# Performance work log

Measured on AMD Instinct MI355X. Metric: run time of the kernel, lower is better.

The kernel has to match this reference:

```python
import jax, jax.numpy as jnp
import numpy as np

B, P, S, D, H, DFF, F, FIN = 16, 25, 1024, 128, 8, 512, 1, 4
SIGMA, OMEGA = 0.1, 0.5
DH = D // H


def setup_inputs() -> dict:
    key = jax.random.key(0)
    ks = jax.random.split(key, 16)
    s = lambda i, sh, sc=1.0: jax.random.normal(ks[i], sh, dtype=jnp.float32) * sc
    return dict(
        x=s(0, (B, P, D)),
        y=s(1, (B, FIN, 1)),
        K=s(2, (B, P, S, D), 0.02),
        V=s(3, (B, P, S, D), 0.02),
        w=jnp.ones((B, P, 1), jnp.float32) / P,
        I=jax.random.randint(ks[4], (B, P, S), 0, P, dtype=jnp.int32),
        Wq=s(5, (D, D), 0.05), Wk=s(6, (D, D), 0.05),
        Wv=s(7, (D, D), 0.05), Wo=s(8, (D, D), 0.05),
        W1=s(9, (D, DFF), 0.05), b1=jnp.zeros((DFF,), jnp.float32),
        W2=s(10, (DFF, D), 0.05), b2=jnp.zeros((D,), jnp.float32),
        Wout=s(11, (D, F), 0.05), bout=jnp.zeros((F,), jnp.float32),
        eps_k=s(12, (B, P, 1, D)), eps_v=s(13, (B, P, 1, D)), eps_z=s(14, (B, P, 1, D)),
        t=512,
    )


def reference(x, y, K, V, w, I, Wq, Wk, Wv, Wo, W1, b1, W2, b2, Wout, bout,
              eps_k, eps_v, eps_z, t):
    # ---- MultiHeadAttention_SMC: per-particle self-attention with reparam noise ----
    xq = x[:, :, None, :]                                   # (B,P,1,D)
    q = xq @ Wq                                             # (B,P,1,D)
    k = xq @ Wk + SIGMA * eps_k                             # noisy key particle
    v = xq @ Wv + SIGMA * eps_v                             # noisy value particle
    K = K.at[:, :, t, :].set(k[:, :, 0, :])                 # write current step into state
    V = V.at[:, :, t, :].set(v[:, :, 0, :])
    q_h = q.reshape(B, P, 1, H, DH)
    K_h = K.reshape(B, P, S, H, DH)
    V_h = V.reshape(B, P, S, H, DH)
    scores = jnp.einsum('bpqhd,bpshd->bphqs', q_h, K_h) / jnp.sqrt(jnp.float32(DH))
    valid = (jnp.arange(S) <= t)[None, None, None, None, :]  # attend to steps <= t
    scores = jnp.where(valid, scores, jnp.float32(-1e9))
    attn = jax.nn.softmax(scores, axis=-1)                  # (B,P,H,1,S)
    ctx = jnp.einsum('bphqs,bpshd->bpqhd', attn, V_h).reshape(B, P, 1, D)
    z = ctx @ Wo + SIGMA * eps_z                            # reparametrized attention output

    # ---- FFN + output layer (dropout is identity at inference) ----
    r_ = jax.nn.relu(z @ W1 + b1) @ W2 + b2                 # (B,P,1,D)
    pred = r_ @ Wout + bout                                 # (B,P,1,F)

    p_t = pred[:, :, 0, :]                                  # (B,P,F)
    y_sq = y[..., 0]                                        # (B,FIN)
    y_t = jnp.broadcast_to(y_sq[:, None, 0:1], (B, P, F))   # target_feature = 0
    mu = y_t - p_t                                          # (B,P,F)
    log_w_full = jnp.einsum('bpf,bqf->bpq', mu, mu) * (-0.5 * OMEGA)
    log_w = jnp.diagonal(log_w_full, axis1=1, axis2=2)      # (B,P)
    log_w = log_w - jnp.min(log_w, axis=-1, keepdims=True)
    w_new = jnp.exp(log_w)
    w_new = w_new / jnp.sum(w_new, axis=1, keepdims=True)
    w_new = jax.lax.stop_gradient(w_new)

    # ---- particle resampling: categorical sample + gather on particle axis ----
    idx = jax.random.categorical(jax.random.key(42),
                                 jnp.log(w_new + 1e-10)[:, None, :],
                                 axis=-1, shape=(B, P))     # (B,P) ancestor indices
    K_res = jnp.take_along_axis(K, idx[:, :, None, None], axis=1)
    V_res = jnp.take_along_axis(V, idx[:, :, None, None], axis=1)
    I_res = jnp.take_along_axis(I, idx[:, :, None], axis=1)
    I_new = I_res.at[:, :, t].set(idx.astype(I.dtype))
    return (r_, z, pred, w_new[..., None], K_res, V_res, I_new)
```

## Files before the change

kernel.cpp:

```cpp
#include <hip/hip_runtime.h>
#include <math.h>

#define B_ 16
#define P_ 25
#define S_ 1024
#define D_ 128
#define H_ 8
#define DH_ 16
#define DFF_ 512
#define SIGMA_ 0.1f


__global__ __launch_bounds__(128) void qkv_kernel(
    const float* __restrict__ x, const float* __restrict__ Wq,
    const float* __restrict__ Wk, const float* __restrict__ Wv,
    const float* __restrict__ eps_k, const float* __restrict__ eps_v,
    float* __restrict__ q, float* __restrict__ k, float* __restrict__ v) {
  int bp = blockIdx.x;
  int d = threadIdx.x;
  __shared__ float xs[D_];
  xs[d] = x[bp * D_ + d];
  __syncthreads();
  float accq = 0.f, acck = 0.f, accv = 0.f;
  for (int i = 0; i < D_; ++i) {
    float xv = xs[i];
    accq += xv * Wq[i * D_ + d];
    acck += xv * Wk[i * D_ + d];
    accv += xv * Wv[i * D_ + d];
  }
  q[bp * D_ + d] = accq;
  k[bp * D_ + d] = acck + SIGMA_ * eps_k[bp * D_ + d];
  v[bp * D_ + d] = accv + SIGMA_ * eps_v[bp * D_ + d];
}

__global__ __launch_bounds__(512) void attn_kernel(
    const float* __restrict__ q, const float* __restrict__ kn,
    const float* __restrict__ vn, const float* __restrict__ K,
    const float* __restrict__ V, const int* __restrict__ tptr,
    float* __restrict__ ctx) {
  int bp = blockIdx.x;
  int t = tptr[0];
  int tid = threadIdx.x;
  int wave = tid >> 6;
  int lane = tid & 63;
  __shared__ float qs[D_];
  __shared__ float accs[8][D_];
  __shared__ float ms[8][H_];
  __shared__ float ls[8][H_];
  if (tid < D_) qs[tid] = q[bp * D_ + tid] * 0.25f;
  __syncthreads();
  const float* Kb = K + (size_t)bp * S_ * D_;
  const float* Vb = V + (size_t)bp * S_ * D_;
  float m = -1e30f, l = 0.f, a0 = 0.f, a1 = 0.f;
  float q0 = qs[2 * lane], q1 = qs[2 * lane + 1];
  for (int s = wave; s <= t; s += 8) {
    const float* Kr, *Vr;
    if (s == t) { Kr = kn + bp * D_; Vr = vn + bp * D_; }
    else        { Kr = Kb + (size_t)s * D_; Vr = Vb + (size_t)s * D_; }
    float2 kk = *(const float2*)(Kr + 2 * lane);
    float2 vv = *(const float2*)(Vr + 2 * lane);
    float p = q0 * kk.x + q1 * kk.y;
    p += __shfl_xor(p, 1);
    p += __shfl_xor(p, 2);
    p += __shfl_xor(p, 4);
    float mnew = fmaxf(m, p);
    float scale = expf(m - mnew);
    float e = expf(p - mnew);
    l = l * scale + e;
    a0 = a0 * scale + e * vv.x;
    a1 = a1 * scale + e * vv.y;
    m = mnew;
  }
  accs[wave][2 * lane] = a0;
  accs[wave][2 * lane + 1] = a1;
  if ((lane & 7) == 0) { ms[wave][lane >> 3] = m; ls[wave][lane >> 3] = l; }
  __syncthreads();
  if (tid < D_) {
    int h = tid >> 4;
    float mg = -1e30f;
    for (int w2 = 0; w2 < 8; ++w2) mg = fmaxf(mg, ms[w2][h]);
    float L = 0.f, C = 0.f;
    for (int w2 = 0; w2 < 8; ++w2) {
      float sc = expf(ms[w2][h] - mg);
      L += ls[w2][h] * sc;
      C += accs[w2][tid] * sc;
    }
    ctx[bp * D_ + tid] = C / L;
  }
}

__global__ __launch_bounds__(512) void head_kernel(
    const float* __restrict__ ctx, const float* __restrict__ Wo,
    const float* __restrict__ eps_z, const float* __restrict__ W1,
    const float* __restrict__ b1, const float* __restrict__ W2,
    const float* __restrict__ b2, const float* __restrict__ Wout,
    const float* __restrict__ bout, float* __restrict__ out_r,
    float* __restrict__ out_z, float* __restrict__ out_pred) {
  int bp = blockIdx.x;
  int tid = threadIdx.x;
  __shared__ float cs[D_];
  __shared__ float zs[D_];
  __shared__ float as[DFF_];
  __shared__ float rs[D_];
  if (tid < D_) cs[tid] = ctx[bp * D_ + tid];
  __syncthreads();
  if (tid < D_) {
    float acc = 0.f;
    for (int i = 0; i < D_; ++i) acc += cs[i] * Wo[i * D_ + tid];
    acc += SIGMA_ * eps_z[bp * D_ + tid];
    zs[tid] = acc;
    out_z[bp * D_ + tid] = acc;
  }
  __syncthreads();
  {
    float acc = b1[tid];
    for (int i = 0; i < D_; ++i) acc += zs[i] * W1[i * DFF_ + tid];
    as[tid] = fmaxf(acc, 0.f);
  }
  __syncthreads();
  if (tid < D_) {
    float acc = b2[tid];
    for (int j = 0; j < DFF_; ++j) acc += as[j] * W2[j * D_ + tid];
    rs[tid] = acc;
    out_r[bp * D_ + tid] = acc;
  }
  __syncthreads();
  if (tid < 64) {
    float acc = rs[tid] * Wout[tid] + rs[tid + 64] * Wout[tid + 64];
    acc += __shfl_xor(acc, 1);
    acc += __shfl_xor(acc, 2);
    acc += __shfl_xor(acc, 4);
    acc += __shfl_xor(acc, 8);
    acc += __shfl_xor(acc, 16);
    acc += __shfl_xor(acc, 32);
    if (tid == 0) out_pred[bp] = acc + bout[0];
  }
}

__device__ inline unsigned rotl_(unsigned x, int r) {
  return (x << r) | (x >> (32 - r));
}

__device__ inline void threefry2x32_(unsigned x0, unsigned x1, unsigned& o0,
                                     unsigned& o1) {
  const unsigned k0 = 0u, k1 = 42u;
  const unsigned k2 = k0 ^ k1 ^ 0x1BD11BDAu;
  x0 += k0; x1 += k1;
#define RND_(r) { x0 += x1; x1 = rotl_(x1, r); x1 ^= x0; }
  RND_(13) RND_(15) RND_(26) RND_(6)   x0 += k1; x1 += k2 + 1u;
  RND_(17) RND_(29) RND_(16) RND_(24)  x0 += k2; x1 += k0 + 2u;
  RND_(13) RND_(15) RND_(26) RND_(6)   x0 += k0; x1 += k1 + 3u;
  RND_(17) RND_(29) RND_(16) RND_(24)  x0 += k1; x1 += k2 + 4u;
  RND_(13) RND_(15) RND_(26) RND_(6)   x0 += k2; x1 += k0 + 5u;
#undef RND_
  o0 = x0; o1 = x1;
}

__device__ inline float gumbel_at_(int n) {
  unsigned o0, o1;
  threefry2x32_(0u, (unsigned)n, o0, o1);
  unsigned bits = o0 ^ o1;
  unsigned fb = (bits >> 9) | 0x3f800000u;
  float f = __uint_as_float(fb) - 1.0f;
  const float tiny = 1.1754944e-38f;
  float u = fmaxf(tiny, f * (1.0f - tiny) + tiny);
  return -logf(-logf(u));
}

__global__ __launch_bounds__(64) void sample_kernel(
    const float* __restrict__ pred, const float* __restrict__ y,
    float* __restrict__ out_w, int* __restrict__ idx) {
  int b = blockIdx.x;
  int tid = threadIdx.x;
  __shared__ float lw[P_];
  __shared__ float logits[P_];
  __shared__ float red[2];
  if (tid < P_) {
    float mu = y[b * 4] - pred[b * P_ + tid];
    lw[tid] = -0.25f * (mu * mu);
  }
  __syncthreads();
  if (tid == 0) {
    float mn = lw[0];
    for (int p = 1; p < P_; ++p) mn = fminf(mn, lw[p]);
    red[0] = mn;
  }
  __syncthreads();
  if (tid < P_) lw[tid] = expf(lw[tid] - red[0]);
  __syncthreads();
  if (tid == 0) {
    float s = 0.f;
    for (int p = 0; p < P_; ++p) s += lw[p];
    red[1] = s;
  }
  __syncthreads();
  if (tid < P_) {
    float wn = lw[tid] / red[1];
    out_w[b * P_ + tid] = wn;
    logits[tid] = logf(wn + 1e-10f);
  }
  __syncthreads();
  if (tid < P_) {
    float best = -1e30f;
    int bestj = 0;
    for (int j = 0; j < P_; ++j) {
      int n = (b * P_ + tid) * P_ + j;
      float val = gumbel_at_(n) + logits[j];
      if (val > best) { best = val; bestj = j; }
    }
    idx[b * P_ + tid] = bestj;
  }
}

__global__ __launch_bounds__(256) void gather_kernel(
    const float* __restrict__ K, const float* __restrict__ V,
    const float* __restrict__ kn, const float* __restrict__ vn,
    const int* __restrict__ idx, const int* __restrict__ tptr,
    float* __restrict__ outK, float* __restrict__ outV) {
  const int CH = 4;
  const int F4 = (S_ * D_ / 4) / CH;
  int bid = blockIdx.x;
  int tv = bid / (B_ * P_ * CH);
  int rem = bid - tv * (B_ * P_ * CH);
  int bp = rem / CH;
  int chunk = rem - bp * CH;
  int b = bp / P_;
  int j = idx[bp];
  int t = tptr[0];
  const float* src = (tv == 0 ? K : V) + (size_t)(b * P_ + j) * (S_ * D_);
  const float4* sub = (const float4*)((tv == 0 ? kn : vn) + (b * P_ + j) * D_);
  float* dst = (tv == 0 ? outK : outV) + (size_t)bp * (S_ * D_);
  const float4* src4 = (const float4*)src;
  float4* dst4 = (float4*)dst;
  int base = chunk * F4;
  int tlo = t * (D_ / 4);
  for (int i = base + threadIdx.x; i < base + F4; i += 256) {
    float4 val;
    if (i >= tlo && i < tlo + D_ / 4) val = sub[i - tlo];
    else                              val = src4[i];
    dst4[i] = val;
  }
}

__global__ __launch_bounds__(256) void inew_kernel(
    const int* __restrict__ I, const int* __restrict__ idx,
    const int* __restrict__ tptr, float* __restrict__ outI) {
  int bp = blockIdx.x;
  int b = bp / P_;
  int j = idx[bp];
  int t = tptr[0];
  const int* src = I + (b * P_ + j) * S_;
  float* dst = outI + bp * S_;
  for (int s = threadIdx.x; s < S_; s += 256) {
    int val = (s == t) ? j : src[s];
    dst[s] = (float)val;
  }
}

extern "C" void kernel_launch(void* const* d_in, const int* in_sizes, int n_in,
                              void* d_out, int out_size, void* d_ws,
                              size_t ws_size, hipStream_t stream) {
  const float* x     = (const float*)d_in[0];
  const float* y     = (const float*)d_in[1];
  const float* K     = (const float*)d_in[2];
  const float* V     = (const float*)d_in[3];
  const int*   I     = (const int*)d_in[5];
  const float* Wq    = (const float*)d_in[6];
  const float* Wk    = (const float*)d_in[7];
  const float* Wv    = (const float*)d_in[8];
  const float* Wo    = (const float*)d_in[9];
  const float* W1    = (const float*)d_in[10];
  const float* b1    = (const float*)d_in[11];
  const float* W2    = (const float*)d_in[12];
  const float* b2    = (const float*)d_in[13];
  const float* Wout  = (const float*)d_in[14];
  const float* bout  = (const float*)d_in[15];
  const float* eps_k = (const float*)d_in[16];
  const float* eps_v = (const float*)d_in[17];
  const float* eps_z = (const float*)d_in[18];
  const int*   tptr  = (const int*)d_in[19];

  float* out      = (float*)d_out;
  float* out_r    = out;
  float* out_z    = out + 51200;
  float* out_pred = out + 102400;
  float* out_w    = out + 102800;
  float* outK     = out + 103200;
  float* outV     = outK + (size_t)52428800;
  float* outI     = outV + (size_t)52428800;

  float* ws  = (float*)d_ws;
  float* q   = ws;
  float* k   = ws + 51200;
  float* v   = ws + 102400;
  float* ctx = ws + 153600;
  int*   idx = (int*)(ws + 204800);

  qkv_kernel<<<B_ * P_, 128, 0, stream>>>(x, Wq, Wk, Wv, eps_k, eps_v, q, k, v);
  attn_kernel<<<B_ * P_, 512, 0, stream>>>(q, k, v, K, V, tptr, ctx);
  head_kernel<<<B_ * P_, 512, 0, stream>>>(ctx, Wo, eps_z, W1, b1, W2, b2, Wout,
                                           bout, out_r, out_z, out_pred);
  sample_kernel<<<B_, 64, 0, stream>>>(out_pred, y, out_w, idx);
  gather_kernel<<<B_ * P_ * 4 * 2, 256, 0, stream>>>(K, V, k, v, idx, tptr,
                                                     outK, outV);
  inew_kernel<<<B_ * P_, 256, 0, stream>>>(I, idx, tptr, outI);
}
```

Measured before the change: 792.6 us.

## Vectorize attention loads, split head matvecs, use nontemporal stores in gather

The attention kernel now loads K/V rows as float4 with half-waves, so each wave processes two sequence rows per iteration and there are sixteen partial softmax states to merge instead of eight. The head kernel splits the Wo and W2 matvecs across all 512 threads with partial sums reduced through shared memory. The gather and I-copy kernels use nontemporal stores to avoid polluting cache with the large K/V resample output. The changes are independent and mainly target memory bandwidth on the copy-dominated path.

```diff
diff --git a/kernel.cpp b/kernel.cpp
--- a/kernel.cpp
+++ b/kernel.cpp
@@ -9,6 +9,8 @@
 #define DH_ 16
 #define DFF_ 512
 #define SIGMA_ 0.1f
+
+typedef float f4 __attribute__((ext_vector_type(4)));
 
 
 __global__ __launch_bounds__(128) void qkv_kernel(
@@ -43,44 +45,51 @@
   int tid = threadIdx.x;
   int wave = tid >> 6;
   int lane = tid & 63;
-  __shared__ float qs[D_];
-  __shared__ float accs[8][D_];
-  __shared__ float ms[8][H_];
-  __shared__ float ls[8][H_];
+  int row = lane >> 5;
+  int lr = lane & 31;
+  int w16 = wave * 2 + row;
+  __shared__ __align__(16) float qs[D_];
+  __shared__ __align__(16) float accs[16][D_];
+  __shared__ float ms[16][H_];
+  __shared__ float ls[16][H_];
   if (tid < D_) qs[tid] = q[bp * D_ + tid] * 0.25f;
   __syncthreads();
-  const float* Kb = K + (size_t)bp * S_ * D_;
-  const float* Vb = V + (size_t)bp * S_ * D_;
-  float m = -1e30f, l = 0.f, a0 = 0.f, a1 = 0.f;
-  float q0 = qs[2 * lane], q1 = qs[2 * lane + 1];
-  for (int s = wave; s <= t; s += 8) {
-    const float* Kr, *Vr;
-    if (s == t) { Kr = kn + bp * D_; Vr = vn + bp * D_; }
-    else        { Kr = Kb + (size_t)s * D_; Vr = Vb + (size_t)s * D_; }
-    float2 kk = *(const float2*)(Kr + 2 * lane);
-    float2 vv = *(const float2*)(Vr + 2 * lane);
-    float p = q0 * kk.x + q1 * kk.y;
+  const f4* Kb = (const f4*)(K + (size_t)bp * S_ * D_);
+  const f4* Vb = (const f4*)(V + (size_t)bp * S_ * D_);
+  const f4* kn4 = (const f4*)(kn + bp * D_);
+  const f4* vn4 = (const f4*)(vn + bp * D_);
+  f4 qv = *(const f4*)(qs + 4 * lr);
+  float m = -1e30f, l = 0.f;
+  f4 acc = {0.f, 0.f, 0.f, 0.f};
+  const int RD4 = D_ / 4;
+  for (int s = w16; s <= t; s += 16) {
+    const f4 *Kr, *Vr;
+    if (s == t) { Kr = kn4; Vr = vn4; }
+    else        { Kr = Kb + (size_t)s * RD4; Vr = Vb + (size_t)s * RD4; }
+    f4 kk = Kr[lr];
+    f4 vv = Vr[lr];
+    float p = qv.x * kk.x + qv.y * kk.y + qv.z * kk.z + qv.w * kk.w;
     p += __shfl_xor(p, 1);
     p += __shfl_xor(p, 2);
-    p += __shfl_xor(p, 4);
     float mnew = fmaxf(m, p);
     float scale = expf(m - mnew);
     float e = expf(p - mnew);
     l = l * scale + e;
-    a0 = a0 * scale + e * vv.x;
-    a1 = a1 * scale + e * vv.y;
+    acc.x = acc.x * scale + e * vv.x;
+    acc.y = acc.y * scale + e * vv.y;
+    acc.z = acc.z * scale + e * vv.z;
+    acc.w = acc.w * scale + e * vv.w;
     m = mnew;
   }
-  accs[wave][2 * lane] = a0;
-  accs[wave][2 * lane + 1] = a1;
-  if ((lane & 7) == 0) { ms[wave][lane >> 3] = m; ls[wave][lane >> 3] = l; }
+  *(f4*)(&accs[w16][4 * lr]) = acc;
+  if ((lr & 3) == 0) { ms[w16][lr >> 2] = m; ls[w16][lr >> 2] = l; }
   __syncthreads();
   if (tid < D_) {
     int h = tid >> 4;
     float mg = -1e30f;
-    for (int w2 = 0; w2 < 8; ++w2) mg = fmaxf(mg, ms[w2][h]);
+    for (int w2 = 0; w2 < 16; ++w2) mg = fmaxf(mg, ms[w2][h]);
     float L = 0.f, C = 0.f;
-    for (int w2 = 0; w2 < 8; ++w2) {
+    for (int w2 = 0; w2 < 16; ++w2) {
       float sc = expf(ms[w2][h] - mg);
       L += ls[w2][h] * sc;
       C += accs[w2][tid] * sc;
@@ -98,31 +107,46 @@
     float* __restrict__ out_z, float* __restrict__ out_pred) {
   int bp = blockIdx.x;
   int tid = threadIdx.x;
+  int d = tid & 127;
+  int qq = tid >> 7;
   __shared__ float cs[D_];
   __shared__ float zs[D_];
-  __shared__ float as[DFF_];
+  __shared__ float as_[DFF_];
   __shared__ float rs[D_];
+  __shared__ float part[4][D_];
   if (tid < D_) cs[tid] = ctx[bp * D_ + tid];
   __syncthreads();
+  {
+    float acc = 0.f;
+    int i0 = qq * 32;
+    for (int i = i0; i < i0 + 32; ++i) acc += cs[i] * Wo[i * D_ + d];
+    part[qq][d] = acc;
+  }
+  __syncthreads();
   if (tid < D_) {
-    float acc = 0.f;
-    for (int i = 0; i < D_; ++i) acc += cs[i] * Wo[i * D_ + tid];
-    acc += SIGMA_ * eps_z[bp * D_ + tid];
-    zs[tid] = acc;
-    out_z[bp * D_ + tid] = acc;
+    float z = part[0][tid] + part[1][tid] + part[2][tid] + part[3][tid] +
+              SIGMA_ * eps_z[bp * D_ + tid];
+    zs[tid] = z;
+    out_z[bp * D_ + tid] = z;
   }
   __syncthreads();
   {
     float acc = b1[tid];
     for (int i = 0; i < D_; ++i) acc += zs[i] * W1[i * DFF_ + tid];
-    as[tid] = fmaxf(acc, 0.f);
+    as_[tid] = fmaxf(acc, 0.f);
+  }
+  __syncthreads();
+  {
+    float acc = 0.f;
+    int j0 = qq * 128;
+    for (int j = j0; j < j0 + 128; ++j) acc += as_[j] * W2[j * D_ + d];
+    part[qq][d] = acc;
   }
   __syncthreads();
   if (tid < D_) {
-    float acc = b2[tid];
-    for (int j = 0; j < DFF_; ++j) acc += as[j] * W2[j * D_ + tid];
-    rs[tid] = acc;
-    out_r[bp * D_ + tid] = acc;
+    float r = part[0][tid] + part[1][tid] + part[2][tid] + part[3][tid] + b2[tid];
+    rs[tid] = r;
+    out_r[bp * D_ + tid] = r;
   }
   __syncthreads();
   if (tid < 64) {
@@ -228,17 +252,17 @@
   int j = idx[bp];
   int t = tptr[0];
   const float* src = (tv == 0 ? K : V) + (size_t)(b * P_ + j) * (S_ * D_);
-  const float4* sub = (const float4*)((tv == 0 ? kn : vn) + (b * P_ + j) * D_);
+  const f4* sub = (const f4*)((tv == 0 ? kn : vn) + (b * P_ + j) * D_);
   float* dst = (tv == 0 ? outK : outV) + (size_t)bp * (S_ * D_);
-  const float4* src4 = (const float4*)src;
-  float4* dst4 = (float4*)dst;
+  const f4* src4 = (const f4*)src;
+  f4* dst4 = (f4*)dst;
   int base = chunk * F4;
   int tlo = t * (D_ / 4);
   for (int i = base + threadIdx.x; i < base + F4; i += 256) {
-    float4 val;
+    f4 val;
     if (i >= tlo && i < tlo + D_ / 4) val = sub[i - tlo];
     else                              val = src4[i];
-    dst4[i] = val;
+    __builtin_nontemporal_store(val, dst4 + i);
   }
 }
 
@@ -253,7 +277,7 @@
   float* dst = outI + bp * S_;
   for (int s = threadIdx.x; s < S_; s += 256) {
     int val = (s == t) ? j : src[s];
-    dst[s] = (float)val;
+    __builtin_nontemporal_store((float)val, dst + s);
   }
 }
 
```

Result: slower. 814.5 us (+2.8%).
